# Kernel tuning notes

Measured on AMD Instinct MI355X. Metric: run time of the kernel, lower is better.

The kernel has to match this reference:

```python
import jax, jax.numpy as jnp
import numpy as np

VAR0, VAR1 = 0.1, 0.2      # cfg['variance'] (standard SSD)
CONF_THRESH = 0.01
TOP_K = 200


def setup_inputs() -> dict:
    key = jax.random.key(0)
    k1, k2, k3 = jax.random.split(key, 3)
    B, P, C = 8, 25575, 81
    return {
        "loc_data": jax.random.normal(k1, (B, P, 4), jnp.float32),
        "conf_data": jax.random.uniform(k2, (B, P, C), jnp.float32),
        "prior_data": jax.random.uniform(k3, (1, P, 4), jnp.float32),
    }


def _decode(loc, priors):
    # SSD box decode: loc [B,P,4], priors [P,4] (cx, cy, w, h)
    centers = priors[..., :2] + loc[..., :2] * VAR0 * priors[..., 2:]
    wh = priors[..., 2:] * jnp.exp(loc[..., 2:] * VAR1)
    mins = centers - wh * 0.5
    return jnp.concatenate([mins, mins + wh], axis=-1)  # [B,P,4] xyxy


def reference(loc_data, conf_data, prior_data):
    priors = prior_data[0]                       # [P,4]
    B, P, C = conf_data.shape
    K = TOP_K
    decoded = _decode(loc_data, priors)          # [B,P,4]
    scores = jnp.transpose(conf_data, (0, 2, 1))  # [B,C,P]
    mask = scores > CONF_THRESH                  # strict gt, as in torch .gt()
    counts = mask.sum(-1)                        # [B,C]

    # --- case B: count > top_k -> keep top_k, sorted descending (torch.topk) ---
    masked = jnp.where(mask, scores, -jnp.inf)
    vals, idx = jax.lax.top_k(masked, K)         # [B,C,K]
    boxes_g = jnp.take_along_axis(decoded[:, None], idx[..., None], axis=2)  # [B,C,K,4]
    valid = vals > CONF_THRESH
    outB = jnp.where(valid[..., None],
                     jnp.concatenate([vals[..., None], boxes_g], axis=-1),
                     0.0)

    # --- case A: count <= top_k -> passing priors in original prior order ---
    entry = jnp.concatenate(
        [scores[..., None], jnp.broadcast_to(decoded[:, None], (B, C, P, 4))], axis=-1)  # [B,C,P,5]
    pos = jnp.where(mask, jnp.cumsum(mask, axis=-1) - 1, K)  # invalid -> dump slot K
    bi = jnp.arange(B)[:, None, None]
    ci = jnp.arange(C)[None, :, None]
    outA = jnp.zeros((B, C, K + 1, 5), scores.dtype).at[bi, ci, pos].set(entry)[:, :, :K]

    return jnp.where((counts <= K)[..., None, None], outA, outB)  # [B,C,K,5]
```

## Files before the change

kernel.cpp:

```cpp
#include <hip/hip_runtime.h>

namespace {

constexpr int B_ = 8;
constexpr int P_ = 25575;
constexpr int C_ = 81;
constexpr int K_ = 200;
constexpr int ROWS = B_ * C_;
constexpr int PC = P_ * C_;
constexpr int EPB = 10368;
constexpr int NB = (PC + EPB - 1) / EPB;
constexpr int NBP = 256;
constexpr int WPR = 800;
constexpr float CONF_T = 0.01f;
constexpr float PREF = 0.9875f;
constexpr float FALLBACK_T = 0.98f;
constexpr int SCAP = 1024;


__global__ __launch_bounds__(256) void scan_k(const float* __restrict__ conf,
                                              unsigned* __restrict__ bmG,
                                              int* __restrict__ cntF_g) {
  __shared__ unsigned bm[C_][4];
  __shared__ int cntF[C_];

  const int b = blockIdx.y;
  const int nb = blockIdx.x;
  const int tid = threadIdx.x;
  const int s = nb * EPB;
  const int e = (s + EPB < PC) ? s + EPB : PC;
  const int pbase = nb * 128;

  for (int i = tid; i < C_ * 4; i += 256) bm[i >> 2][i & 3] = 0u;
  for (int i = tid; i < C_; i += 256) cntF[i] = 0;
  __syncthreads();

  const float* cb = conf + (size_t)b * PC;

  auto process = [&](int L, float f) {
    bool isC = (f > PREF);
    bool isF = !(f > CONF_T);
    if (!isC && !isF) return;
    unsigned p = (unsigned)L / 81u;
    unsigned c = (unsigned)L - p * 81u;
    if (isC) {
      unsigned pl = p - pbase;
      atomicOr(&bm[c][pl >> 5], 1u << (pl & 31));
    } else {
      atomicAdd(&cntF[c], 1);
    }
  };

  const int a0 = s + (b & 3);
  const int n4 = (e - a0) >> 2;
  const int a1 = a0 + (n4 << 2);

  for (int L = s + tid; L < a0; L += 256) process(L, cb[L]);
  const float4* c4 = reinterpret_cast<const float4*>(conf) + (((size_t)b * PC + a0) >> 2);
  for (int k = tid; k < n4; k += 256) {
    float4 q = c4[k];
    float mx = fmaxf(fmaxf(q.x, q.y), fmaxf(q.z, q.w));
    float mn = fminf(fminf(q.x, q.y), fminf(q.z, q.w));
    if ((mx > PREF) || !(mn > CONF_T)) {
      int L = a0 + (k << 2);
      process(L + 0, q.x);
      process(L + 1, q.y);
      process(L + 2, q.z);
      process(L + 3, q.w);
    }
  }
  for (int L = a1 + tid; L < e; L += 256) process(L, cb[L]);

  __syncthreads();
  for (int i = tid; i < C_; i += 256)
    cntF_g[(b * C_ + i) * NBP + nb] = cntF[i];
  for (int i = tid; i < C_ * 4; i += 256) {
    int c = i >> 2, w = i & 3;
    bmG[(size_t)(b * C_ + c) * WPR + nb * 4 + w] = bm[c][w];
  }
}

__global__ __launch_bounds__(256) void select_k(const float* __restrict__ conf,
                                                const float* __restrict__ loc,
                                                const float* __restrict__ prior,
                                                const unsigned* __restrict__ bmG,
                                                const int* __restrict__ cntF_g,
                                                float* __restrict__ out) {
  __shared__ alignas(16) unsigned long long skey[SCAP];
  __shared__ unsigned short clist[SCAP];
  __shared__ int wtot[4];
  __shared__ int ftot[4];
  __shared__ int spart[256];
  __shared__ int scnt;

  const int row = blockIdx.x;
  const int b = row / C_;
  const int c = row - b * C_;
  const int tid = threadIdx.x;
  const int lane = tid & 63;
  const int wid = tid >> 6;
  const size_t obase = (size_t)row * K_ * 5;

  uint4 w4 = make_uint4(0u, 0u, 0u, 0u);
  int cnt = 0;
  if (tid < NB) {
    w4 = reinterpret_cast<const uint4*>(bmG + (size_t)row * WPR)[tid];
    cnt = __popc(w4.x) + __popc(w4.y) + __popc(w4.z) + __popc(w4.w);
  }
  int incl = cnt;
  for (int o = 1; o < 64; o <<= 1) {
    int v = __shfl_up(incl, o);
    if (lane >= o) incl += v;
  }
  if (lane == 63) wtot[wid] = incl;
  int f = 0;
  if (tid < NB) f = cntF_g[row * NBP + tid];
  for (int o = 32; o; o >>= 1) f += __shfl_down(f, o);
  if (lane == 0) ftot[wid] = f;
  __syncthreads();

  int wbase = 0;
  for (int k = 0; k < wid; ++k) wbase += wtot[k];
  const int nAll = wtot[0] + wtot[1] + wtot[2] + wtot[3];
  const int fail = ftot[0] + ftot[1] + ftot[2] + ftot[3];

  if (cnt > 0) {
    int base = wbase + incl - cnt;
    int p0 = tid << 7;
    unsigned wv[4] = {w4.x, w4.y, w4.z, w4.w};
#pragma unroll
    for (int w = 0; w < 4; ++w) {
      unsigned x = wv[w];
      while (x) {
        int bit = __ffs(x) - 1;
        x &= x - 1;
        if (base < SCAP) clist[base] = (unsigned short)(p0 + (w << 5) + bit);
        ++base;
      }
    }
  }
  __syncthreads();

  const bool ovf = (nAll > SCAP);
  int n = ovf ? SCAP : nAll;
  const int count = P_ - fail;
  const bool caseA = (count <= K_);
  const bool fb = (!caseA) && (ovf || n < K_);

  auto decode_store = [&](unsigned long long ki, int rank, bool swapKey) {
    unsigned p, vb;
    if (swapKey) {
      p = ~(unsigned)(ki >> 32);
      vb = (unsigned)ki;
    } else {
      vb = (unsigned)(ki >> 32);
      p = ~(unsigned)ki;
    }
    float4 l4 = reinterpret_cast<const float4*>(loc)[(size_t)b * P_ + p];
    float4 pr = reinterpret_cast<const float4*>(prior)[p];
    float cx = pr.x + l4.x * 0.1f * pr.z;
    float cy = pr.y + l4.y * 0.1f * pr.w;
    float w = pr.z * expf(l4.z * 0.2f);
    float h = pr.w * expf(l4.w * 0.2f);
    float x1 = cx - w * 0.5f;
    float y1 = cy - h * 0.5f;
    const size_t o = obase + (size_t)rank * 5;
    out[o + 0] = __uint_as_float(vb);
    out[o + 1] = x1;
    out[o + 2] = y1;
    out[o + 3] = x1 + w;
    out[o + 4] = y1 + h;
  };

  if (caseA || fb) {
    const bool useA = caseA;
    const float thr = useA ? CONF_T : ((count < SCAP) ? CONF_T : FALLBACK_T);
    if (tid == 0) scnt = 0;
    __syncthreads();
    for (int p = tid; p < P_; p += 256) {
      float fv = conf[((size_t)b * P_ + p) * C_ + c];
      if (fv > thr) {
        int pos = atomicAdd(&scnt, 1);
        if (pos < SCAP) {
          skey[pos] = useA
              ? (((unsigned long long)(~(unsigned)p) << 32) |
                 (unsigned long long)__float_as_uint(fv))
              : (((unsigned long long)__float_as_uint(fv) << 32) |
                 (unsigned long long)(~(unsigned)p));
        }
      }
    }
    __syncthreads();
    int n2 = scnt < SCAP ? scnt : SCAP;
    const int nPad = (n2 + 7) & ~7;
    for (int i = n2 + tid; i < nPad; i += 256) skey[i] = 0ull;
    __syncthreads();
    const int n_out = (n2 < K_) ? n2 : K_;
    for (int s2 = n_out * 5 + tid; s2 < K_ * 5; s2 += 256) out[obase + s2] = 0.f;
    const ulonglong2* k2 = reinterpret_cast<const ulonglong2*>(skey);
    const int nPairs = nPad >> 1;
    for (int i = tid; i < n2; i += 256) {
      const unsigned long long ki = skey[i];
      int rank = 0;
      for (int j = 0; j + 3 < nPairs; j += 4) {
        ulonglong2 a = k2[j], bq = k2[j + 1], cq = k2[j + 2], dq = k2[j + 3];
        rank += (a.x > ki) + (a.y > ki) + (bq.x > ki) + (bq.y > ki) +
                (cq.x > ki) + (cq.y > ki) + (dq.x > ki) + (dq.y > ki);
      }
      for (int j = nPairs & ~3; j < nPairs; ++j) {
        ulonglong2 a = k2[j];
        rank += (a.x > ki) + (a.y > ki);
      }
      if (rank < K_) decode_store(ki, rank, useA);
    }
    return;
  }

  for (int i = tid; i < n; i += 256) {
    int p = clist[i];
    float fv = conf[(size_t)b * PC + (size_t)p * C_ + c];
    skey[i] = ((unsigned long long)__float_as_uint(fv) << 32) |
              (unsigned long long)(~(unsigned)p);
  }
  const int nPad = (n + 31) & ~31;
  for (int i = n + tid; i < nPad; i += 256) skey[i] = 0ull;
  __syncthreads();

  const int nPairs = nPad >> 1;
  const int CP = nPairs >> 2;
  const ulonglong2* k2 = reinterpret_cast<const ulonglong2*>(skey);

  for (int kb = 0; kb < n; kb += 64) {
    const int ki_idx = kb + lane;
    const unsigned long long ki = (ki_idx < n) ? skey[ki_idx] : ~0ull;
    int part = 0;
    const int c0 = wid * CP;
    const int c1 = c0 + CP;
    for (int j = c0; j < c1; j += 4) {
      ulonglong2 a = k2[j], bq = k2[j + 1], cq = k2[j + 2], dq = k2[j + 3];
      part += (a.x > ki) + (a.y > ki) + (bq.x > ki) + (bq.y > ki) +
              (cq.x > ki) + (cq.y > ki) + (dq.x > ki) + (dq.y > ki);
    }
    spart[tid] = part;
    __syncthreads();
    if (tid < 64) {
      const int idx2 = kb + tid;
      if (idx2 < n) {
        const unsigned long long k = skey[idx2];
        const int rank = spart[tid] + spart[tid + 64] + spart[tid + 128] +
                         spart[tid + 192];
        if (rank < K_) decode_store(k, rank, false);
      }
    }
    __syncthreads();
  }
}

}

extern "C" void kernel_launch(void* const* d_in, const int* in_sizes, int n_in,
                              void* d_out, int out_size, void* d_ws, size_t ws_size,
                              hipStream_t stream) {
  const float* loc = (const float*)d_in[0];
  const float* conf = (const float*)d_in[1];
  const float* prior = (const float*)d_in[2];
  float* out = (float*)d_out;

  unsigned* bmG = (unsigned*)d_ws;
  int* cntF_g = (int*)(bmG + (size_t)ROWS * WPR);

  dim3 grid1(NB, B_);
  scan_k<<<grid1, 256, 0, stream>>>(conf, bmG, cntF_g);
  select_k<<<ROWS, 256, 0, stream>>>(conf, loc, prior, bmG, cntF_g, out);
}
```

Before: 40.18 us.

## Fuse scan and select kernels into one persistent kernel with grid barrier

Merges the scan and select kernels into a single launch of 800 blocks. Each block first processes scan slices, then waits at a global atomic-counter barrier before doing the per-row select work. This removes the second kernel launch and the gap between the two kernels. In exchange it adds a memset, a spin barrier that relies on all 800 blocks being co-resident (launch_bounds 256,4), and a guarded timeout that could let blocks proceed early.

```diff
diff --git a/kernel.cpp b/kernel.cpp
--- a/kernel.cpp
+++ b/kernel.cpp
@@ -9,7 +9,9 @@
 constexpr int ROWS = B_ * C_;
 constexpr int PC = P_ * C_;
 constexpr int EPB = 10368;
-constexpr int NB = (PC + EPB - 1) / EPB;
+constexpr int NB = 200;
+constexpr int SLICES = NB * B_;
+constexpr int NBLK = 800;
 constexpr int NBP = 256;
 constexpr int WPR = 800;
 constexpr float CONF_T = 0.01f;
@@ -18,74 +20,13 @@
 constexpr int SCAP = 1024;
 
 
-__global__ __launch_bounds__(256) void scan_k(const float* __restrict__ conf,
-                                              unsigned* __restrict__ bmG,
-                                              int* __restrict__ cntF_g) {
+__global__ __launch_bounds__(256, 4) void fused_k(
+    const float* __restrict__ conf, const float* __restrict__ loc,
+    const float* __restrict__ prior, unsigned* __restrict__ bmG,
+    int* __restrict__ cntF_g, unsigned* __restrict__ bar,
+    float* __restrict__ out) {
   __shared__ unsigned bm[C_][4];
   __shared__ int cntF[C_];
-
-  const int b = blockIdx.y;
-  const int nb = blockIdx.x;
-  const int tid = threadIdx.x;
-  const int s = nb * EPB;
-  const int e = (s + EPB < PC) ? s + EPB : PC;
-  const int pbase = nb * 128;
-
-  for (int i = tid; i < C_ * 4; i += 256) bm[i >> 2][i & 3] = 0u;
-  for (int i = tid; i < C_; i += 256) cntF[i] = 0;
-  __syncthreads();
-
-  const float* cb = conf + (size_t)b * PC;
-
-  auto process = [&](int L, float f) {
-    bool isC = (f > PREF);
-    bool isF = !(f > CONF_T);
-    if (!isC && !isF) return;
-    unsigned p = (unsigned)L / 81u;
-    unsigned c = (unsigned)L - p * 81u;
-    if (isC) {
-      unsigned pl = p - pbase;
-      atomicOr(&bm[c][pl >> 5], 1u << (pl & 31));
-    } else {
-      atomicAdd(&cntF[c], 1);
-    }
-  };
-
-  const int a0 = s + (b & 3);
-  const int n4 = (e - a0) >> 2;
-  const int a1 = a0 + (n4 << 2);
-
-  for (int L = s + tid; L < a0; L += 256) process(L, cb[L]);
-  const float4* c4 = reinterpret_cast<const float4*>(conf) + (((size_t)b * PC + a0) >> 2);
-  for (int k = tid; k < n4; k += 256) {
-    float4 q = c4[k];
-    float mx = fmaxf(fmaxf(q.x, q.y), fmaxf(q.z, q.w));
-    float mn = fminf(fminf(q.x, q.y), fminf(q.z, q.w));
-    if ((mx > PREF) || !(mn > CONF_T)) {
-      int L = a0 + (k << 2);
-      process(L + 0, q.x);
-      process(L + 1, q.y);
-      process(L + 2, q.z);
-      process(L + 3, q.w);
-    }
-  }
-  for (int L = a1 + tid; L < e; L += 256) process(L, cb[L]);
-
-  __syncthreads();
-  for (int i = tid; i < C_; i += 256)
-    cntF_g[(b * C_ + i) * NBP + nb] = cntF[i];
-  for (int i = tid; i < C_ * 4; i += 256) {
-    int c = i >> 2, w = i & 3;
-    bmG[(size_t)(b * C_ + c) * WPR + nb * 4 + w] = bm[c][w];
-  }
-}
-
-__global__ __launch_bounds__(256) void select_k(const float* __restrict__ conf,
-                                                const float* __restrict__ loc,
-                                                const float* __restrict__ prior,
-                                                const unsigned* __restrict__ bmG,
-                                                const int* __restrict__ cntF_g,
-                                                float* __restrict__ out) {
   __shared__ alignas(16) unsigned long long skey[SCAP];
   __shared__ unsigned short clist[SCAP];
   __shared__ int wtot[4];
@@ -93,12 +34,86 @@
   __shared__ int spart[256];
   __shared__ int scnt;
 
-  const int row = blockIdx.x;
-  const int b = row / C_;
-  const int c = row - b * C_;
   const int tid = threadIdx.x;
   const int lane = tid & 63;
   const int wid = tid >> 6;
+
+  for (int sl = blockIdx.x; sl < SLICES; sl += NBLK) {
+    const int b = sl & 7;
+    const int nb = sl >> 3;
+    const int s = nb * EPB;
+    const int e = (s + EPB < PC) ? s + EPB : PC;
+    const int pbase = nb * 128;
+
+    for (int i = tid; i < C_ * 4; i += 256) bm[i >> 2][i & 3] = 0u;
+    for (int i = tid; i < C_; i += 256) cntF[i] = 0;
+    __syncthreads();
+
+    const float* cb = conf + (size_t)b * PC;
+
+    auto process = [&](int L, float f) {
+      bool isC = (f > PREF);
+      bool isF = !(f > CONF_T);
+      if (!isC && !isF) return;
+      unsigned p = (unsigned)L / 81u;
+      unsigned c = (unsigned)L - p * 81u;
+      if (isC) {
+        unsigned pl = p - pbase;
+        atomicOr(&bm[c][pl >> 5], 1u << (pl & 31));
+      } else {
+        atomicAdd(&cntF[c], 1);
+      }
+    };
+
+    const int a0 = s + (b & 3);
+    const int n4 = (e - a0) >> 2;
+    const int a1 = a0 + (n4 << 2);
+
+    for (int L = s + tid; L < a0; L += 256) process(L, cb[L]);
+    const float4* c4 =
+        reinterpret_cast<const float4*>(conf) + (((size_t)b * PC + a0) >> 2);
+    for (int k = tid; k < n4; k += 256) {
+      float4 q = c4[k];
+      float mx = fmaxf(fmaxf(q.x, q.y), fmaxf(q.z, q.w));
+      float mn = fminf(fminf(q.x, q.y), fminf(q.z, q.w));
+      if ((mx > PREF) || !(mn > CONF_T)) {
+        int L = a0 + (k << 2);
+        process(L + 0, q.x);
+        process(L + 1, q.y);
+        process(L + 2, q.z);
+        process(L + 3, q.w);
+      }
+    }
+    for (int L = a1 + tid; L < e; L += 256) process(L, cb[L]);
+
+    __syncthreads();
+    for (int i = tid; i < C_; i += 256)
+      cntF_g[(b * C_ + i) * NBP + nb] = cntF[i];
+    for (int i = tid; i < C_ * 4; i += 256) {
+      int c = i >> 2, w = i & 3;
+      bmG[(size_t)(b * C_ + c) * WPR + nb * 4 + w] = bm[c][w];
+    }
+    __syncthreads();
+  }
+
+  __syncthreads();
+  if (tid == 0) {
+    __threadfence();
+    atomicAdd(bar, 1u);
+    long guard = 0;
+    while (__hip_atomic_load(bar, __ATOMIC_RELAXED, __HIP_MEMORY_SCOPE_AGENT) <
+           (unsigned)NBLK) {
+      __builtin_amdgcn_s_sleep(8);
+      if (++guard > (1L << 26)) break;
+    }
+    __threadfence();
+  }
+  __syncthreads();
+
+  const int row = blockIdx.x;
+  if (row >= ROWS) return;
+  const int b = row / C_;
+  const int c = row - b * C_;
   const size_t obase = (size_t)row * K_ * 5;
 
   uint4 w4 = make_uint4(0u, 0u, 0u, 0u);
@@ -268,8 +283,8 @@
 
   unsigned* bmG = (unsigned*)d_ws;
   int* cntF_g = (int*)(bmG + (size_t)ROWS * WPR);
-
-  dim3 grid1(NB, B_);
-  scan_k<<<grid1, 256, 0, stream>>>(conf, bmG, cntF_g);
-  select_k<<<ROWS, 256, 0, stream>>>(conf, loc, prior, bmG, cntF_g, out);
+  unsigned* bar = (unsigned*)(cntF_g + ROWS * NBP);
+
+  hipMemsetAsync(bar, 0, sizeof(unsigned), stream);
+  fused_k<<<NBLK, 256, 0, stream>>>(conf, loc, prior, bmG, cntF_g, bar, out);
 }
```

Measured after the change: 135.6 us. 3.38x slower.
